# Performance work log

Measured on AMD Instinct MI355X. Metric: run time of the kernel, lower is better.

## Reference

```python
import jax, jax.numpy as jnp
import numpy as np

N = 50000       # nodes
E = 800000      # edges (before self-loops)
IN = 64         # in_channels
OUT = 64        # out_channels


def setup_inputs() -> dict:
    key = jax.random.key(0)
    ks = jax.random.split(key, 6)
    X = jax.random.normal(ks[0], (N, IN), jnp.float32)
    H = jax.random.normal(ks[1], (N, OUT), jnp.float32)
    edge_index = jax.random.randint(ks[2], (2, E), 0, N, dtype=jnp.int64)
    edge_weight = jax.random.uniform(ks[3], (E,), jnp.float32)
    fan_in = IN + OUT
    W1 = jax.random.normal(ks[4], (fan_in, 2 * OUT), jnp.float32) / np.sqrt(fan_in).astype(np.float32)
    b1 = jnp.ones((2 * OUT,), jnp.float32)   # TGCN sets graph_conv1.bias to ones
    W2 = jax.random.normal(ks[5], (fan_in, OUT), jnp.float32) / np.sqrt(fan_in).astype(np.float32)
    b2 = jnp.zeros((OUT,), jnp.float32)      # default GCNConv bias init
    return {"X": X, "H": H, "edge_index": edge_index, "edge_weight": edge_weight,
            "W1": W1, "b1": b1, "W2": W2, "b2": b2}


def _gcn_conv(x, W, b, src, dst, w, n):
    """PyG GCNConv: linear transform, add self-loops (fill=1, improved=False),
    symmetric deg^-1/2 normalization, scatter-add aggregation at dst, + bias."""
    x = x @ W                                   # [N, out]
    loop = jnp.arange(n, dtype=src.dtype)
    s = jnp.concatenate([src, loop])            # [E+N]
    d = jnp.concatenate([dst, loop])
    ww = jnp.concatenate([w, jnp.ones((n,), x.dtype)])
    deg = jax.ops.segment_sum(ww, d, num_segments=n)
    dinv = jnp.where(deg > 0, jax.lax.rsqrt(jnp.maximum(deg, 1e-12)), 0.0)
    norm = dinv[s] * ww * dinv[d]               # [E+N]
    msg = x[s] * norm[:, None]                  # gather + scale
    out = jax.ops.segment_sum(msg, d, num_segments=n)  # scatter-add at dst
    return out + b


def reference(X, H, edge_index, edge_weight, W1, b1, W2, b2):
    src, dst = edge_index[0], edge_index[1]
    n = X.shape[0]
    ru = jax.nn.sigmoid(_gcn_conv(jnp.concatenate([X, H], axis=1), W1, b1, src, dst, edge_weight, n))
    r, u = ru[:, :OUT], ru[:, OUT:]             # chunk into reset/update gates
    c = jnp.tanh(_gcn_conv(jnp.concatenate([X, H * r], axis=1), W2, b2, src, dst, edge_weight, n))
    return u * H + (1.0 - u) * c                # new hidden state [N, OUT]
```

## Files before the change

kernel.cpp:

```cpp
#include <hip/hip_runtime.h>
#include <hip/hip_bf16.h>
#include <hip/hip_fp16.h>

#define NN 50000
#define NE 800000
#define NBIN ((NN + 255) / 256)
#define PB ((NE + 1023) / 1024)
#define GB ((NN + 63) / 64)
#define MAXB 4864

typedef __attribute__((ext_vector_type(8))) short bf16x8;
typedef __attribute__((ext_vector_type(4))) float f32x4;
typedef __attribute__((ext_vector_type(2))) float f32x2;

__device__ __forceinline__ unsigned int f2bf(float x) {
    unsigned int u = __float_as_uint(x);
    return (u + 0x7FFFu + ((u >> 16) & 1u)) >> 16;
}
__device__ __forceinline__ float bf2f(unsigned int b) {
    return __uint_as_float(b << 16);
}
__device__ __forceinline__ float4 f8x4_dec(unsigned int u) {
    f32x2 lo = __builtin_amdgcn_cvt_pk_f32_fp8(u, false);
    f32x2 hi = __builtin_amdgcn_cvt_pk_f32_fp8(u, true);
    float4 r; r.x = lo[0]; r.y = lo[1]; r.z = hi[0]; r.w = hi[1];
    return r;
}
__device__ __forceinline__ unsigned int f8x4_enc(float a, float b, float c, float d) {
    int q = 0;
    q = __builtin_amdgcn_cvt_pk_fp8_f32(a, b, q, false);
    q = __builtin_amdgcn_cvt_pk_fp8_f32(c, d, q, true);
    return (unsigned int)q;
}

__global__ void k_wprep(const float* __restrict__ W1, const float* __restrict__ W2,
                        unsigned short* __restrict__ Wf1,
                        unsigned short* __restrict__ Wf2t,
                        unsigned short* __restrict__ Wf2b) {
    int i = blockIdx.x * 256 + threadIdx.x;
    if (i < 16384) {
        int j = i & 7, l = (i >> 3) & 63, n = (i >> 9) & 7, kc = i >> 12;
        int k = kc * 32 + ((l >> 4) << 3) + j;
        int col = (n << 4) + (l & 15);
        Wf1[i] = (unsigned short)f2bf(W1[k * 128 + col]);
    }
    if (i < 4096) {
        int j = i & 7, l = (i >> 3) & 63, n = (i >> 9) & 3, kc = i >> 11;
        int k = kc * 32 + ((l >> 4) << 3) + j;
        int col = (n << 4) + (l & 15);
        Wf2t[i] = (unsigned short)f2bf(W2[k * 64 + col]);
        Wf2b[i] = (unsigned short)f2bf(W2[(k + 64) * 64 + col]);
    }
}

template <int OUTC, int KC, int SRC, int OMODE>
__device__ __forceinline__ void mgemm_core(
    const float* __restrict__ X, const float* __restrict__ Hm,
    const unsigned int* __restrict__ RUb, const unsigned short* __restrict__ Wf,
    const float* __restrict__ Z2p, const float* __restrict__ dinv,
    unsigned short* __restrict__ outH, float* __restrict__ outF,
    int bid, unsigned short* aS, unsigned short* wS)
{
    constexpr int NT = OUTC / 16;
    const int tid = threadIdx.x;
    const int row0 = bid * 64;

    constexpr int WH = KC * NT * 64 * 8;
    {
        const uint4* Wg4 = reinterpret_cast<const uint4*>(Wf);
        uint4* wS4 = reinterpret_cast<uint4*>(wS);
        #pragma unroll
        for (int i = tid; i < WH / 8; i += 256) wS4[i] = Wg4[i];
    }
    #pragma unroll
    for (int i = tid; i < 64 * KC * 8; i += 256) {
        int row = i / (KC * 8), f4 = i % (KC * 8);
        int g = row0 + row;
        float4 v = {0.f, 0.f, 0.f, 0.f};
        if (g < NN) {
            if (SRC == 0) {
                v = (f4 < 16) ? reinterpret_cast<const float4*>(X)[g * 16 + f4]
                              : reinterpret_cast<const float4*>(Hm)[g * 16 + f4 - 16];
            } else if (SRC == 1) {
                v = reinterpret_cast<const float4*>(X)[g * 16 + f4];
            } else {
                v = reinterpret_cast<const float4*>(Hm)[g * 16 + f4];
                unsigned int r0 = RUb[g * 64 + 2 * f4];
                unsigned int r1 = RUb[g * 64 + 2 * f4 + 1];
                v.x *= bf2f(r0 & 0xFFFFu); v.y *= bf2f(r0 >> 16);
                v.z *= bf2f(r1 & 0xFFFFu); v.w *= bf2f(r1 >> 16);
            }
        }
        int k = f4 * 4;
        int kc = k >> 5, ko = k & 31;
        int l = (row & 15) | ((ko >> 3) << 4);
        int j0 = ko & 7;
        int m = row >> 4;
        uint2 pk;
        pk.x = f2bf(v.x) | (f2bf(v.y) << 16);
        pk.y = f2bf(v.z) | (f2bf(v.w) << 16);
        *reinterpret_cast<uint2*>(aS + (((m * KC + kc) * 64 + l) * 8 + j0)) = pk;
    }
    __syncthreads();

    const int wid = tid >> 6, l = tid & 63;
    f32x4 acc[NT];
    #pragma unroll
    for (int n = 0; n < NT; ++n) acc[n] = {0.f, 0.f, 0.f, 0.f};

    const bf16x8* aF = reinterpret_cast<const bf16x8*>(aS);
    const bf16x8* wF = reinterpret_cast<const bf16x8*>(wS);
    #pragma unroll
    for (int kc = 0; kc < KC; ++kc) {
        bf16x8 a = aF[(wid * KC + kc) * 64 + l];
        #pragma unroll
        for (int n = 0; n < NT; ++n) {
            bf16x8 b = wF[(kc * NT + n) * 64 + l];
            acc[n] = __builtin_amdgcn_mfma_f32_16x16x32_bf16(a, b, acc[n], 0, 0, 0);
        }
    }

    const int rbase = row0 + wid * 16 + ((l >> 4) << 2);
    const int cl = l & 15;
    float dv[4];
    if (OMODE == 2) {
        #pragma unroll
        for (int i = 0; i < 4; ++i) {
            int row = rbase + i;
            dv[i] = (row < NN) ? dinv[row] : 0.f;
        }
    }
    #pragma unroll
    for (int n = 0; n < NT; ++n) {
        #pragma unroll
        for (int i = 0; i < 4; ++i) {
            int row = rbase + i;
            if (row >= NN) continue;
            int col = n * 16 + cl;
            if (OMODE == 0) {
                outH[(size_t)row * OUTC + col] = (unsigned short)f2bf(acc[n][i]);
            } else if (OMODE == 1) {
                outF[(size_t)row * OUTC + col] = acc[n][i];
            } else {
                float a2 = (acc[n][i] + Z2p[(size_t)row * 64 + col]) * dv[i];
                outH[(size_t)row * 64 + col] = (unsigned short)f2bf(a2);
            }
        }
    }
}

__launch_bounds__(256)
__global__ void k_build(const float* __restrict__ X, const float* __restrict__ Hm,
                        const unsigned short* __restrict__ Wf1,
                        const unsigned short* __restrict__ Wf2t,
                        unsigned short* __restrict__ Z1b, float* __restrict__ Z2p,
                        const int* __restrict__ dst, int* __restrict__ HT) {
    __shared__ unsigned short aS[8192];
    __shared__ unsigned short wS[16384];
    const int bid = blockIdx.x;
    const int tid = threadIdx.x;
    if (bid < PB) {
        int* hist = reinterpret_cast<int*>(aS);
        for (int i = tid; i < NBIN; i += 256) hist[i] = 0;
        __syncthreads();
        const int base = bid * 1024 + tid;
        #pragma unroll
        for (int k = 0; k < 4; ++k) {
            int e = base + k * 256;
            if (e < NE) atomicAdd(&hist[dst[e] >> 8], 1);
        }
        __syncthreads();
        for (int i = tid; i < NBIN; i += 256) HT[i * PB + bid] = hist[i];
        return;
    }
    if (bid < PB + GB) {
        mgemm_core<128, 4, 0, 0>(X, Hm, nullptr, Wf1, nullptr, nullptr,
                                 Z1b, nullptr, bid - PB, aS, wS);
        return;
    }
    mgemm_core<64, 2, 1, 1>(X, Hm, nullptr, Wf2t, nullptr, nullptr,
                            nullptr, Z2p, bid - PB - GB, aS, wS);
}

__launch_bounds__(256)
__global__ void k_gemm2b(const float* __restrict__ X, const float* __restrict__ Hm,
                         const unsigned int* __restrict__ RUb,
                         const unsigned short* __restrict__ Wf2b,
                         const float* __restrict__ Z2p, const float* __restrict__ dinv,
                         unsigned short* __restrict__ Z2b) {
    __shared__ unsigned short aS[4096];
    __shared__ unsigned short wS[4096];
    mgemm_core<64, 2, 2, 2>(X, Hm, RUb, Wf2b, Z2p, dinv, Z2b, nullptr,
                            blockIdx.x, aS, wS);
}

__launch_bounds__(256)
__global__ void k_scanA1(const int* __restrict__ HT, int* __restrict__ within,
                         int* __restrict__ binTot) {
    __shared__ int lds[PB];
    __shared__ int sc[256];
    __shared__ int carryS;
    const int b = blockIdx.x, tid = threadIdx.x;
    if (tid == 0) carryS = 0;
    for (int i = tid; i < PB; i += 256) lds[i] = HT[b * PB + i];
    __syncthreads();
    for (int c0 = 0; c0 < PB; c0 += 256) {
        int i = c0 + tid;
        int v = (i < PB) ? lds[i] : 0;
        sc[tid] = v;
        __syncthreads();
        #pragma unroll
        for (int off = 1; off < 256; off <<= 1) {
            int t = (tid >= off) ? sc[tid - off] : 0;
            __syncthreads();
            sc[tid] += t;
            __syncthreads();
        }
        int carry = carryS;
        if (i < PB) lds[i] = carry + sc[tid] - v;
        __syncthreads();
        if (tid == 255) carryS = carry + sc[255];
        __syncthreads();
    }
    for (int i = tid; i < PB; i += 256) within[b * PB + i] = lds[i];
    if (tid == 0) binTot[b] = carryS;
}

__launch_bounds__(256)
__global__ void k_scatterA(const int* __restrict__ src, const int* __restrict__ dst,
                           const float* __restrict__ w, const int* __restrict__ binTot,
                           const int* __restrict__ within, uint2* __restrict__ rec) {
    __shared__ int bS[256];
    __shared__ int cur[NBIN];
    const int blk = blockIdx.x, tid = threadIdx.x;
    int bv = (tid < NBIN) ? binTot[tid] : 0;
    bS[tid] = bv;
    __syncthreads();
    #pragma unroll
    for (int off = 1; off < 256; off <<= 1) {
        int t = (tid >= off) ? bS[tid - off] : 0;
        __syncthreads();
        bS[tid] += t;
        __syncthreads();
    }
    if (tid < NBIN) cur[tid] = (bS[tid] - bv) + within[tid * PB + blk];
    __syncthreads();
    const int base = blk * 1024 + tid;
    #pragma unroll
    for (int k = 0; k < 4; ++k) {
        int e = base + k * 256;
        if (e < NE) {
            int d = dst[e];
            int pos = atomicAdd(&cur[d >> 8], 1);
            unsigned int hn = __half_as_ushort(__float2half(w[e]));
            uint2 r;
            r.x = (unsigned int)src[e] | (hn << 16);
            r.y = (unsigned int)d;
            rec[pos] = r;
        }
    }
}

__launch_bounds__(256)
__global__ void k_phase2(const uint2* __restrict__ rec, const int* __restrict__ binTot,
                         unsigned int* __restrict__ snP, int* __restrict__ start,
                         float* __restrict__ dinv, const uint2* __restrict__ Z1b,
                         unsigned int* __restrict__ Zf8) {
    __shared__ unsigned int rSn[MAXB];
    __shared__ unsigned char rLo[MAXB];
    __shared__ unsigned int outSn[MAXB];
    __shared__ int cnt[256];
    __shared__ int sc[256];
    __shared__ int lstart[256];
    __shared__ int cur[256];
    __shared__ float dls[256];
    const int b = blockIdx.x, tid = threadIdx.x;

    int bv = (tid < NBIN) ? binTot[tid] : 0;
    sc[tid] = bv;
    __syncthreads();
    #pragma unroll
    for (int off = 1; off < 256; off <<= 1) {
        int t = (tid >= off) ? sc[tid - off] : 0;
        __syncthreads();
        sc[tid] += t;
        __syncthreads();
    }
    const int e0 = (b == 0) ? 0 : sc[b - 1];
    int nE = sc[b] - e0;
    __syncthreads();
    if (nE > MAXB) nE = MAXB;

    cnt[tid] = 0;
    __syncthreads();
    for (int i = tid; i < nE; i += 256) {
        uint2 r = rec[e0 + i];
        rSn[i] = r.x;
        int lo = r.y & 255;
        rLo[i] = (unsigned char)lo;
        atomicAdd(&cnt[lo], 1);
    }
    __syncthreads();
    sc[tid] = cnt[tid];
    __syncthreads();
    #pragma unroll
    for (int off = 1; off < 256; off <<= 1) {
        int t = (tid >= off) ? sc[tid - off] : 0;
        __syncthreads();
        sc[tid] += t;
        __syncthreads();
    }
    lstart[tid] = sc[tid] - cnt[tid];
    cur[tid] = sc[tid] - cnt[tid];
    __syncthreads();
    const int node = b * 256 + tid;
    if (node <= NN) start[node] = e0 + lstart[tid];
    for (int i = tid; i < nE; i += 256) {
        int p = atomicAdd(&cur[rLo[i]], 1);
        outSn[p] = rSn[i];
    }
    __syncthreads();
    for (int i = tid; i < nE; i += 256) snP[e0 + i] = outSn[i];
    {
        int s0 = lstart[tid], c = cnt[tid];
        float sum = 0.f;
        for (int i = s0; i < s0 + c; ++i)
            sum += __half2float(__ushort_as_half((unsigned short)(outSn[i] >> 16)));
        float dv = rsqrtf(1.0f + sum);
        dls[tid] = dv;
        if (node < NN) dinv[node] = dv;
    }
    __syncthreads();
    const int nLoc = (NN - b * 256 < 256) ? (NN - b * 256) : 256;
    for (int i = tid; i < nLoc * 32; i += 256) {
        int l = i >> 5, j = i & 31;
        size_t g = (size_t)(b * 256 + l) * 32 + j;
        uint2 z = Z1b[g];
        float dv = dls[l];
        Zf8[g] = f8x4_enc(bf2f(z.x & 0xFFFFu) * dv, bf2f(z.x >> 16) * dv,
                          bf2f(z.y & 0xFFFFu) * dv, bf2f(z.y >> 16) * dv);
    }
}

__launch_bounds__(256)
__global__ void k_gather1(const int* __restrict__ start, const unsigned int* __restrict__ snP,
                          const unsigned int* __restrict__ Zf8, const float* __restrict__ dinv,
                          const float* __restrict__ bias, uint2* __restrict__ RUb2) {
    const int node = blockIdx.x * 8 + (threadIdx.x >> 5);
    const int l = threadIdx.x & 31;
    if (node >= NN) return;

    const int e0 = start[node], e1 = start[node + 1];
    float4 acc = f8x4_dec(Zf8[(size_t)node * 32 + l]);

    #define EFMA8(U, NM) { float4 zz = f8x4_dec(U); \
        acc.x += zz.x * (NM); acc.y += zz.y * (NM); \
        acc.z += zz.z * (NM); acc.w += zz.w * (NM); }

    int e = e0;
    for (; e + 8 <= e1; e += 8) {
        unsigned sn0 = snP[e],     sn1 = snP[e + 1], sn2 = snP[e + 2], sn3 = snP[e + 3];
        unsigned sn4 = snP[e + 4], sn5 = snP[e + 5], sn6 = snP[e + 6], sn7 = snP[e + 7];
        unsigned z0 = Zf8[(size_t)(sn0 & 0xFFFFu) * 32 + l];
        unsigned z1 = Zf8[(size_t)(sn1 & 0xFFFFu) * 32 + l];
        unsigned z2 = Zf8[(size_t)(sn2 & 0xFFFFu) * 32 + l];
        unsigned z3 = Zf8[(size_t)(sn3 & 0xFFFFu) * 32 + l];
        unsigned z4 = Zf8[(size_t)(sn4 & 0xFFFFu) * 32 + l];
        unsigned z5 = Zf8[(size_t)(sn5 & 0xFFFFu) * 32 + l];
        unsigned z6 = Zf8[(size_t)(sn6 & 0xFFFFu) * 32 + l];
        unsigned z7 = Zf8[(size_t)(sn7 & 0xFFFFu) * 32 + l];
        float n0 = __half2float(__ushort_as_half((unsigned short)(sn0 >> 16)));
        float n1 = __half2float(__ushort_as_half((unsigned short)(sn1 >> 16)));
        float n2 = __half2float(__ushort_as_half((unsigned short)(sn2 >> 16)));
        float n3 = __half2float(__ushort_as_half((unsigned short)(sn3 >> 16)));
        float n4 = __half2float(__ushort_as_half((unsigned short)(sn4 >> 16)));
        float n5 = __half2float(__ushort_as_half((unsigned short)(sn5 >> 16)));
        float n6 = __half2float(__ushort_as_half((unsigned short)(sn6 >> 16)));
        float n7 = __half2float(__ushort_as_half((unsigned short)(sn7 >> 16)));
        EFMA8(z0, n0) EFMA8(z1, n1) EFMA8(z2, n2) EFMA8(z3, n3)
        EFMA8(z4, n4) EFMA8(z5, n5) EFMA8(z6, n6) EFMA8(z7, n7)
    }
    if (e + 4 <= e1) {
        unsigned sn0 = snP[e], sn1 = snP[e + 1], sn2 = snP[e + 2], sn3 = snP[e + 3];
        unsigned z0 = Zf8[(size_t)(sn0 & 0xFFFFu) * 32 + l];
        unsigned z1 = Zf8[(size_t)(sn1 & 0xFFFFu) * 32 + l];
        unsigned z2 = Zf8[(size_t)(sn2 & 0xFFFFu) * 32 + l];
        unsigned z3 = Zf8[(size_t)(sn3 & 0xFFFFu) * 32 + l];
        float n0 = __half2float(__ushort_as_half((unsigned short)(sn0 >> 16)));
        float n1 = __half2float(__ushort_as_half((unsigned short)(sn1 >> 16)));
        float n2 = __half2float(__ushort_as_half((unsigned short)(sn2 >> 16)));
        float n3 = __half2float(__ushort_as_half((unsigned short)(sn3 >> 16)));
        EFMA8(z0, n0) EFMA8(z1, n1) EFMA8(z2, n2) EFMA8(z3, n3)
        e += 4;
    }
    for (; e < e1; ++e) {
        unsigned sn = snP[e];
        float nm = __half2float(__ushort_as_half((unsigned short)(sn >> 16)));
        unsigned z = Zf8[(size_t)(sn & 0xFFFFu) * 32 + l];
        EFMA8(z, nm)
    }
    #undef EFMA8

    const float dv = dinv[node];
    const int c = l * 4;
    float4 bb = *reinterpret_cast<const float4*>(bias + c);
    acc.x = acc.x * dv + bb.x; acc.y = acc.y * dv + bb.y;
    acc.z = acc.z * dv + bb.z; acc.w = acc.w * dv + bb.w;

    float4 o;
    o.x = 1.f / (1.f + expf(-acc.x));
    o.y = 1.f / (1.f + expf(-acc.y));
    o.z = 1.f / (1.f + expf(-acc.z));
    o.w = 1.f / (1.f + expf(-acc.w));
    uint2 pk;
    pk.x = f2bf(o.x) | (f2bf(o.y) << 16);
    pk.y = f2bf(o.z) | (f2bf(o.w) << 16);
    RUb2[(size_t)node * 32 + l] = pk;
}

__launch_bounds__(256)
__global__ void k_gather2(const int* __restrict__ start, const unsigned int* __restrict__ snP,
                          const uint2* __restrict__ Zb, const float* __restrict__ dinv,
                          const float* __restrict__ bias, const uint2* __restrict__ RUb2,
                          const float* __restrict__ Hm, float* __restrict__ out) {
    constexpr int GRP = 16;
    const int node = blockIdx.x * 16 + threadIdx.x / GRP;
    const int l = threadIdx.x % GRP;
    if (node >= NN) return;

    const int e0 = start[node], e1 = start[node + 1];

    uint2 zs = Zb[(size_t)node * GRP + l];
    float4 acc;
    acc.x = bf2f(zs.x & 0xFFFFu);
    acc.y = bf2f(zs.x >> 16);
    acc.z = bf2f(zs.y & 0xFFFFu);
    acc.w = bf2f(zs.y >> 16);

    #define EFMA(Z, NM) \
        acc.x += bf2f((Z).x & 0xFFFFu) * (NM); \
        acc.y += bf2f((Z).x >> 16) * (NM);     \
        acc.z += bf2f((Z).y & 0xFFFFu) * (NM); \
        acc.w += bf2f((Z).y >> 16) * (NM);

    int e = e0;
    for (; e + 8 <= e1; e += 8) {
        unsigned sn0 = snP[e],     sn1 = snP[e + 1], sn2 = snP[e + 2], sn3 = snP[e + 3];
        unsigned sn4 = snP[e + 4], sn5 = snP[e + 5], sn6 = snP[e + 6], sn7 = snP[e + 7];
        uint2 z0 = Zb[(size_t)(sn0 & 0xFFFFu) * GRP + l];
        uint2 z1 = Zb[(size_t)(sn1 & 0xFFFFu) * GRP + l];
        uint2 z2 = Zb[(size_t)(sn2 & 0xFFFFu) * GRP + l];
        uint2 z3 = Zb[(size_t)(sn3 & 0xFFFFu) * GRP + l];
        uint2 z4 = Zb[(size_t)(sn4 & 0xFFFFu) * GRP + l];
        uint2 z5 = Zb[(size_t)(sn5 & 0xFFFFu) * GRP + l];
        uint2 z6 = Zb[(size_t)(sn6 & 0xFFFFu) * GRP + l];
        uint2 z7 = Zb[(size_t)(sn7 & 0xFFFFu) * GRP + l];
        float n0 = __half2float(__ushort_as_half((unsigned short)(sn0 >> 16)));
        float n1 = __half2float(__ushort_as_half((unsigned short)(sn1 >> 16)));
        float n2 = __half2float(__ushort_as_half((unsigned short)(sn2 >> 16)));
        float n3 = __half2float(__ushort_as_half((unsigned short)(sn3 >> 16)));
        float n4 = __half2float(__ushort_as_half((unsigned short)(sn4 >> 16)));
        float n5 = __half2float(__ushort_as_half((unsigned short)(sn5 >> 16)));
        float n6 = __half2float(__ushort_as_half((unsigned short)(sn6 >> 16)));
        float n7 = __half2float(__ushort_as_half((unsigned short)(sn7 >> 16)));
        EFMA(z0, n0) EFMA(z1, n1) EFMA(z2, n2) EFMA(z3, n3)
        EFMA(z4, n4) EFMA(z5, n5) EFMA(z6, n6) EFMA(z7, n7)
    }
    if (e + 4 <= e1) {
        unsigned sn0 = snP[e], sn1 = snP[e + 1], sn2 = snP[e + 2], sn3 = snP[e + 3];
        uint2 z0 = Zb[(size_t)(sn0 & 0xFFFFu) * GRP + l];
        uint2 z1 = Zb[(size_t)(sn1 & 0xFFFFu) * GRP + l];
        uint2 z2 = Zb[(size_t)(sn2 & 0xFFFFu) * GRP + l];
        uint2 z3 = Zb[(size_t)(sn3 & 0xFFFFu) * GRP + l];
        float n0 = __half2float(__ushort_as_half((unsigned short)(sn0 >> 16)));
        float n1 = __half2float(__ushort_as_half((unsigned short)(sn1 >> 16)));
        float n2 = __half2float(__ushort_as_half((unsigned short)(sn2 >> 16)));
        float n3 = __half2float(__ushort_as_half((unsigned short)(sn3 >> 16)));
        EFMA(z0, n0) EFMA(z1, n1) EFMA(z2, n2) EFMA(z3, n3)
        e += 4;
    }
    for (; e < e1; ++e) {
        unsigned sn = snP[e];
        float nm = __half2float(__ushort_as_half((unsigned short)(sn >> 16)));
        uint2 z = Zb[(size_t)(sn & 0xFFFFu) * GRP + l];
        EFMA(z, nm)
    }
    #undef EFMA

    const float dv = dinv[node];
    const int c = l * 4;
    float4 bb = *reinterpret_cast<const float4*>(bias + c);
    acc.x = acc.x * dv + bb.x; acc.y = acc.y * dv + bb.y;
    acc.z = acc.z * dv + bb.z; acc.w = acc.w * dv + bb.w;

    uint2 uu = RUb2[(size_t)node * 32 + 16 + l];
    float u0 = bf2f(uu.x & 0xFFFFu), u1 = bf2f(uu.x >> 16);
    float u2 = bf2f(uu.y & 0xFFFFu), u3 = bf2f(uu.y >> 16);
    float4 h4 = *reinterpret_cast<const float4*>(Hm + (size_t)node * 64 + c);
    float4 o;
    o.x = u0 * h4.x + (1.f - u0) * tanhf(acc.x);
    o.y = u1 * h4.y + (1.f - u1) * tanhf(acc.y);
    o.z = u2 * h4.z + (1.f - u2) * tanhf(acc.z);
    o.w = u3 * h4.w + (1.f - u3) * tanhf(acc.w);
    *reinterpret_cast<float4*>(out + (size_t)node * 64 + c) = o;
}

extern "C" void kernel_launch(void* const* d_in, const int* in_sizes, int n_in,
                              void* d_out, int out_size, void* d_ws, size_t ws_size,
                              hipStream_t stream) {
    const float* X  = (const float*)d_in[0];
    const float* Hm = (const float*)d_in[1];
    const int*   ei = (const int*)d_in[2];
    const float* w  = (const float*)d_in[3];
    const float* W1 = (const float*)d_in[4];
    const float* b1 = (const float*)d_in[5];
    const float* W2 = (const float*)d_in[6];
    const float* b2 = (const float*)d_in[7];
    float* out = (float*)d_out;

    const int* src = ei;
    const int* dst = ei + NE;

    char* p = (char*)d_ws;
    uint2* rec   = (uint2*)p;  p += sizeof(uint2) * NE;
    uint2* Z1b   = (uint2*)p;  p += sizeof(uint2) * NN * 32;
    uint2* Z2b   = (uint2*)p;  p += sizeof(uint2) * NN * 16;
    uint2* RUb2  = (uint2*)p;  p += sizeof(uint2) * NN * 32;
    float* Z2p   = (float*)p;  p += sizeof(float) * NN * 64;
    float* dinv  = (float*)p;  p += sizeof(float) * NN;
    int*   start = (int*)p;    p += sizeof(int) * (NN + 1);
    int*   binTot   = (int*)p; p += sizeof(int) * (NBIN + 1);
    int*   HT       = (int*)p; p += sizeof(int) * NBIN * PB;
    int*   within   = (int*)p; p += sizeof(int) * NBIN * PB;
    unsigned int* snP = (unsigned int*)p; p += sizeof(unsigned int) * NE;
    unsigned int* Zf8 = (unsigned int*)p; p += sizeof(unsigned int) * NN * 32;
    unsigned short* Wf1  = (unsigned short*)p; p += sizeof(unsigned short) * 16384;
    unsigned short* Wf2t = (unsigned short*)p; p += sizeof(unsigned short) * 4096;
    unsigned short* Wf2b = (unsigned short*)p; p += sizeof(unsigned short) * 4096;

    k_wprep<<<64, 256, 0, stream>>>(W1, W2, Wf1, Wf2t, Wf2b);

    k_build<<<PB + 2 * GB, 256, 0, stream>>>(X, Hm, Wf1, Wf2t,
                                             (unsigned short*)Z1b, Z2p, dst, HT);

    k_scanA1<<<NBIN, 256, 0, stream>>>(HT, within, binTot);
    k_scatterA<<<PB, 256, 0, stream>>>(src, dst, w, binTot, within, rec);
    k_phase2<<<NBIN, 256, 0, stream>>>(rec, binTot, snP, start, dinv, Z1b, Zf8);

    k_gather1<<<(NN + 7) / 8, 256, 0, stream>>>(start, snP, Zf8, dinv, b1, RUb2);

    k_gemm2b<<<GB, 256, 0, stream>>>(X, Hm, (const unsigned int*)RUb2, Wf2b,
                                     Z2p, dinv, (unsigned short*)Z2b);
    k_gather2<<<(NN + 15) / 16, 256, 0, stream>>>(start, snP, Z2b, dinv, b2, RUb2, Hm, out);
}
```

Before: 122.4 us.

## Write unscaled fp8 Z1 from GEMM and apply source dinv per edge in gathers

```diff
diff --git a/kernel.cpp b/kernel.cpp
--- a/kernel.cpp
+++ b/kernel.cpp
@@ -25,12 +25,6 @@
     f32x2 hi = __builtin_amdgcn_cvt_pk_f32_fp8(u, true);
     float4 r; r.x = lo[0]; r.y = lo[1]; r.z = hi[0]; r.w = hi[1];
     return r;
-}
-__device__ __forceinline__ unsigned int f8x4_enc(float a, float b, float c, float d) {
-    int q = 0;
-    q = __builtin_amdgcn_cvt_pk_fp8_f32(a, b, q, false);
-    q = __builtin_amdgcn_cvt_pk_fp8_f32(c, d, q, true);
-    return (unsigned int)q;
 }
 
 __global__ void k_wprep(const float* __restrict__ W1, const float* __restrict__ W2,
@@ -57,8 +51,9 @@
 __device__ __forceinline__ void mgemm_core(
     const float* __restrict__ X, const float* __restrict__ Hm,
     const unsigned int* __restrict__ RUb, const unsigned short* __restrict__ Wf,
-    const float* __restrict__ Z2p, const float* __restrict__ dinv,
+    const float* __restrict__ addF,
     unsigned short* __restrict__ outH, float* __restrict__ outF,
+    unsigned char* __restrict__ outF8,
     int bid, unsigned short* aS, unsigned short* wS)
 {
     constexpr int NT = OUTC / 16;
@@ -122,14 +117,6 @@
 
     const int rbase = row0 + wid * 16 + ((l >> 4) << 2);
     const int cl = l & 15;
-    float dv[4];
-    if (OMODE == 2) {
-        #pragma unroll
-        for (int i = 0; i < 4; ++i) {
-            int row = rbase + i;
-            dv[i] = (row < NN) ? dinv[row] : 0.f;
-        }
-    }
     #pragma unroll
     for (int n = 0; n < NT; ++n) {
         #pragma unroll
@@ -137,13 +124,14 @@
             int row = rbase + i;
             if (row >= NN) continue;
             int col = n * 16 + cl;
-            if (OMODE == 0) {
-                outH[(size_t)row * OUTC + col] = (unsigned short)f2bf(acc[n][i]);
-            } else if (OMODE == 1) {
+            if (OMODE == 1) {
                 outF[(size_t)row * OUTC + col] = acc[n][i];
+            } else if (OMODE == 2) {
+                float a2 = acc[n][i] + addF[(size_t)row * OUTC + col];
+                outH[(size_t)row * OUTC + col] = (unsigned short)f2bf(a2);
             } else {
-                float a2 = (acc[n][i] + Z2p[(size_t)row * 64 + col]) * dv[i];
-                outH[(size_t)row * 64 + col] = (unsigned short)f2bf(a2);
+                int q = __builtin_amdgcn_cvt_pk_fp8_f32(acc[n][i], acc[n][i], 0, false);
+                outF8[(size_t)row * OUTC + col] = (unsigned char)(q & 0xFF);
             }
         }
     }
@@ -153,7 +141,7 @@
 __global__ void k_build(const float* __restrict__ X, const float* __restrict__ Hm,
                         const unsigned short* __restrict__ Wf1,
                         const unsigned short* __restrict__ Wf2t,
-                        unsigned short* __restrict__ Z1b, float* __restrict__ Z2p,
+                        unsigned char* __restrict__ Zf8, float* __restrict__ Z2p,
                         const int* __restrict__ dst, int* __restrict__ HT) {
     __shared__ unsigned short aS[8192];
     __shared__ unsigned short wS[16384];
@@ -174,23 +162,23 @@
         return;
     }
     if (bid < PB + GB) {
-        mgemm_core<128, 4, 0, 0>(X, Hm, nullptr, Wf1, nullptr, nullptr,
-                                 Z1b, nullptr, bid - PB, aS, wS);
+        mgemm_core<128, 4, 0, 3>(X, Hm, nullptr, Wf1, nullptr,
+                                 nullptr, nullptr, Zf8, bid - PB, aS, wS);
         return;
     }
-    mgemm_core<64, 2, 1, 1>(X, Hm, nullptr, Wf2t, nullptr, nullptr,
-                            nullptr, Z2p, bid - PB - GB, aS, wS);
+    mgemm_core<64, 2, 1, 1>(X, Hm, nullptr, Wf2t, nullptr,
+                            nullptr, Z2p, nullptr, bid - PB - GB, aS, wS);
 }
 
 __launch_bounds__(256)
 __global__ void k_gemm2b(const float* __restrict__ X, const float* __restrict__ Hm,
                          const unsigned int* __restrict__ RUb,
                          const unsigned short* __restrict__ Wf2b,
-                         const float* __restrict__ Z2p, const float* __restrict__ dinv,
+                         const float* __restrict__ Z2p,
                          unsigned short* __restrict__ Z2b) {
     __shared__ unsigned short aS[4096];
     __shared__ unsigned short wS[4096];
-    mgemm_core<64, 2, 2, 2>(X, Hm, RUb, Wf2b, Z2p, dinv, Z2b, nullptr,
+    mgemm_core<64, 2, 2, 2>(X, Hm, RUb, Wf2b, Z2p, Z2b, nullptr, nullptr,
                             blockIdx.x, aS, wS);
 }
 
@@ -264,8 +252,7 @@
 __launch_bounds__(256)
 __global__ void k_phase2(const uint2* __restrict__ rec, const int* __restrict__ binTot,
                          unsigned int* __restrict__ snP, int* __restrict__ start,
-                         float* __restrict__ dinv, const uint2* __restrict__ Z1b,
-                         unsigned int* __restrict__ Zf8) {
+                         float* __restrict__ dinv) {
     __shared__ unsigned int rSn[MAXB];
     __shared__ unsigned char rLo[MAXB];
     __shared__ unsigned int outSn[MAXB];
@@ -273,7 +260,6 @@
     __shared__ int sc[256];
     __shared__ int lstart[256];
     __shared__ int cur[256];
-    __shared__ float dls[256];
     const int b = blockIdx.x, tid = threadIdx.x;
 
     int bv = (tid < NBIN) ? binTot[tid] : 0;
@@ -326,19 +312,7 @@
         float sum = 0.f;
         for (int i = s0; i < s0 + c; ++i)
             sum += __half2float(__ushort_as_half((unsigned short)(outSn[i] >> 16)));
-        float dv = rsqrtf(1.0f + sum);
-        dls[tid] = dv;
-        if (node < NN) dinv[node] = dv;
-    }
-    __syncthreads();
-    const int nLoc = (NN - b * 256 < 256) ? (NN - b * 256) : 256;
-    for (int i = tid; i < nLoc * 32; i += 256) {
-        int l = i >> 5, j = i & 31;
-        size_t g = (size_t)(b * 256 + l) * 32 + j;
-        uint2 z = Z1b[g];
-        float dv = dls[l];
-        Zf8[g] = f8x4_enc(bf2f(z.x & 0xFFFFu) * dv, bf2f(z.x >> 16) * dv,
-                          bf2f(z.y & 0xFFFFu) * dv, bf2f(z.y >> 16) * dv);
+        if (node < NN) dinv[node] = rsqrtf(1.0f + sum);
     }
 }
 
@@ -351,11 +325,15 @@
     if (node >= NN) return;
 
     const int e0 = start[node], e1 = start[node + 1];
+    const float dvd = dinv[node];
     float4 acc = f8x4_dec(Zf8[(size_t)node * 32 + l]);
+    acc.x *= dvd; acc.y *= dvd; acc.z *= dvd; acc.w *= dvd;
 
     #define EFMA8(U, NM) { float4 zz = f8x4_dec(U); \
         acc.x += zz.x * (NM); acc.y += zz.y * (NM); \
         acc.z += zz.z * (NM); acc.w += zz.w * (NM); }
+    #define NMOF(SN) (dinv[(SN) & 0xFFFFu] * \
+        __half2float(__ushort_as_half((unsigned short)((SN) >> 16))))
 
     int e = e0;
     for (; e + 8 <= e1; e += 8) {
@@ -369,14 +347,8 @@
         unsigned z5 = Zf8[(size_t)(sn5 & 0xFFFFu) * 32 + l];
         unsigned z6 = Zf8[(size_t)(sn6 & 0xFFFFu) * 32 + l];
         unsigned z7 = Zf8[(size_t)(sn7 & 0xFFFFu) * 32 + l];
-        float n0 = __half2float(__ushort_as_half((unsigned short)(sn0 >> 16)));
-        float n1 = __half2float(__ushort_as_half((unsigned short)(sn1 >> 16)));
-        float n2 = __half2float(__ushort_as_half((unsigned short)(sn2 >> 16)));
-        float n3 = __half2float(__ushort_as_half((unsigned short)(sn3 >> 16)));
-        float n4 = __half2float(__ushort_as_half((unsigned short)(sn4 >> 16)));
-        float n5 = __half2float(__ushort_as_half((unsigned short)(sn5 >> 16)));
-        float n6 = __half2float(__ushort_as_half((unsigned short)(sn6 >> 16)));
-        float n7 = __half2float(__ushort_as_half((unsigned short)(sn7 >> 16)));
+        float n0 = NMOF(sn0), n1 = NMOF(sn1), n2 = NMOF(sn2), n3 = NMOF(sn3);
+        float n4 = NMOF(sn4), n5 = NMOF(sn5), n6 = NMOF(sn6), n7 = NMOF(sn7);
         EFMA8(z0, n0) EFMA8(z1, n1) EFMA8(z2, n2) EFMA8(z3, n3)
         EFMA8(z4, n4) EFMA8(z5, n5) EFMA8(z6, n6) EFMA8(z7, n7)
     }
@@ -386,26 +358,23 @@
         unsigned z1 = Zf8[(size_t)(sn1 & 0xFFFFu) * 32 + l];
         unsigned z2 = Zf8[(size_t)(sn2 & 0xFFFFu) * 32 + l];
         unsigned z3 = Zf8[(size_t)(sn3 & 0xFFFFu) * 32 + l];
-        float n0 = __half2float(__ushort_as_half((unsigned short)(sn0 >> 16)));
-        float n1 = __half2float(__ushort_as_half((unsigned short)(sn1 >> 16)));
-        float n2 = __half2float(__ushort_as_half((unsigned short)(sn2 >> 16)));
-        float n3 = __half2float(__ushort_as_half((unsigned short)(sn3 >> 16)));
+        float n0 = NMOF(sn0), n1 = NMOF(sn1), n2 = NMOF(sn2), n3 = NMOF(sn3);
         EFMA8(z0, n0) EFMA8(z1, n1) EFMA8(z2, n2) EFMA8(z3, n3)
         e += 4;
     }
     for (; e < e1; ++e) {
         unsigned sn = snP[e];
-        float nm = __half2float(__ushort_as_half((unsigned short)(sn >> 16)));
         unsigned z = Zf8[(size_t)(sn & 0xFFFFu) * 32 + l];
+        float nm = NMOF(sn);
         EFMA8(z, nm)
     }
     #undef EFMA8
-
-    const float dv = dinv[node];
+    #undef NMOF
+
     const int c = l * 4;
     float4 bb = *reinterpret_cast<const float4*>(bias + c);
-    acc.x = acc.x * dv + bb.x; acc.y = acc.y * dv + bb.y;
-    acc.z = acc.z * dv + bb.z; acc.w = acc.w * dv + bb.w;
+    acc.x = acc.x * dvd + bb.x; acc.y = acc.y * dvd + bb.y;
+    acc.z = acc.z * dvd + bb.z; acc.w = acc.w * dvd + bb.w;
 
     float4 o;
     o.x = 1.f / (1.f + expf(-acc.x));
@@ -429,19 +398,22 @@
     if (node >= NN) return;
 
     const int e0 = start[node], e1 = start[node + 1];
+    const float dvd = dinv[node];
 
     uint2 zs = Zb[(size_t)node * GRP + l];
     float4 acc;
-    acc.x = bf2f(zs.x & 0xFFFFu);
-    acc.y = bf2f(zs.x >> 16);
-    acc.z = bf2f(zs.y & 0xFFFFu);
-    acc.w = bf2f(zs.y >> 16);
+    acc.x = bf2f(zs.x & 0xFFFFu) * dvd;
+    acc.y = bf2f(zs.x >> 16) * dvd;
+    acc.z = bf2f(zs.y & 0xFFFFu) * dvd;
+    acc.w = bf2f(zs.y >> 16) * dvd;
 
     #define EFMA(Z, NM) \
         acc.x += bf2f((Z).x & 0xFFFFu) * (NM); \
         acc.y += bf2f((Z).x >> 16) * (NM);     \
         acc.z += bf2f((Z).y & 0xFFFFu) * (NM); \
         acc.w += bf2f((Z).y >> 16) * (NM);
+    #define NMOF(SN) (dinv[(SN) & 0xFFFFu] * \
+        __half2float(__ushort_as_half((unsigned short)((SN) >> 16))))
 
     int e = e0;
     for (; e + 8 <= e1; e += 8) {
@@ -455,14 +427,8 @@
         uint2 z5 = Zb[(size_t)(sn5 & 0xFFFFu) * GRP + l];
         uint2 z6 = Zb[(size_t)(sn6 & 0xFFFFu) * GRP + l];
         uint2 z7 = Zb[(size_t)(sn7 & 0xFFFFu) * GRP + l];
-        float n0 = __half2float(__ushort_as_half((unsigned short)(sn0 >> 16)));
-        float n1 = __half2float(__ushort_as_half((unsigned short)(sn1 >> 16)));
-        float n2 = __half2float(__ushort_as_half((unsigned short)(sn2 >> 16)));
-        float n3 = __half2float(__ushort_as_half((unsigned short)(sn3 >> 16)));
-        float n4 = __half2float(__ushort_as_half((unsigned short)(sn4 >> 16)));
-        float n5 = __half2float(__ushort_as_half((unsigned short)(sn5 >> 16)));
-        float n6 = __half2float(__ushort_as_half((unsigned short)(sn6 >> 16)));
-        float n7 = __half2float(__ushort_as_half((unsigned short)(sn7 >> 16)));
+        float n0 = NMOF(sn0), n1 = NMOF(sn1), n2 = NMOF(sn2), n3 = NMOF(sn3);
+        float n4 = NMOF(sn4), n5 = NMOF(sn5), n6 = NMOF(sn6), n7 = NMOF(sn7);
         EFMA(z0, n0) EFMA(z1, n1) EFMA(z2, n2) EFMA(z3, n3)
         EFMA(z4, n4) EFMA(z5, n5) EFMA(z6, n6) EFMA(z7, n7)
     }
@@ -472,26 +438,23 @@
         uint2 z1 = Zb[(size_t)(sn1 & 0xFFFFu) * GRP + l];
         uint2 z2 = Zb[(size_t)(sn2 & 0xFFFFu) * GRP + l];
         uint2 z3 = Zb[(size_t)(sn3 & 0xFFFFu) * GRP + l];
-        float n0 = __half2float(__ushort_as_half((unsigned short)(sn0 >> 16)));
-        float n1 = __half2float(__ushort_as_half((unsigned short)(sn1 >> 16)));
-        float n2 = __half2float(__ushort_as_half((unsigned short)(sn2 >> 16)));
-        float n3 = __half2float(__ushort_as_half((unsigned short)(sn3 >> 16)));
+        float n0 = NMOF(sn0), n1 = NMOF(sn1), n2 = NMOF(sn2), n3 = NMOF(sn3);
         EFMA(z0, n0) EFMA(z1, n1) EFMA(z2, n2) EFMA(z3, n3)
         e += 4;
     }
     for (; e < e1; ++e) {
         unsigned sn = snP[e];
-        float nm = __half2float(__ushort_as_half((unsigned short)(sn >> 16)));
         uint2 z = Zb[(size_t)(sn & 0xFFFFu) * GRP + l];
+        float nm = NMOF(sn);
         EFMA(z, nm)
     }
     #undef EFMA
-
-    const float dv = dinv[node];
+    #undef NMOF
+
     const int c = l * 4;
     float4 bb = *reinterpret_cast<const float4*>(bias + c);
-    acc.x = acc.x * dv + bb.x; acc.y = acc.y * dv + bb.y;
-    acc.z = acc.z * dv + bb.z; acc.w = acc.w * dv + bb.w;
+    acc.x = acc.x * dvd + bb.x; acc.y = acc.y * dvd + bb.y;
+    acc.z = acc.z * dvd + bb.z; acc.w = acc.w * dvd + bb.w;
 
     uint2 uu = RUb2[(size_t)node * 32 + 16 + l];
     float u0 = bf2f(uu.x & 0xFFFFu), u1 = bf2f(uu.x >> 16);
@@ -523,7 +486,6 @@
 
     char* p = (char*)d_ws;
     uint2* rec   = (uint2*)p;  p += sizeof(uint2) * NE;
-    uint2* Z1b   = (uint2*)p;  p += sizeof(uint2) * NN * 32;
     uint2* Z2b   = (uint2*)p;  p += sizeof(uint2) * NN * 16;
     uint2* RUb2  = (uint2*)p;  p += sizeof(uint2) * NN * 32;
     float* Z2p   = (float*)p;  p += sizeof(float) * NN * 64;
@@ -541,15 +503,15 @@
     k_wprep<<<64, 256, 0, stream>>>(W1, W2, Wf1, Wf2t, Wf2b);
 
     k_build<<<PB + 2 * GB, 256, 0, stream>>>(X, Hm, Wf1, Wf2t,
-                                             (unsigned short*)Z1b, Z2p, dst, HT);
+                                             (unsigned char*)Zf8, Z2p, dst, HT);
 
     k_scanA1<<<NBIN, 256, 0, stream>>>(HT, within, binTot);
     k_scatterA<<<PB, 256, 0, stream>>>(src, dst, w, binTot, within, rec);
-    k_phase2<<<NBIN, 256, 0, stream>>>(rec, binTot, snP, start, dinv, Z1b, Zf8);
+    k_phase2<<<NBIN, 256, 0, stream>>>(rec, binTot, snP, start, dinv);
 
     k_gather1<<<(NN + 7) / 8, 256, 0, stream>>>(start, snP, Zf8, dinv, b1, RUb2);
 
-    k_gemm2b<<<GB, 256, 0, stream>>>(X, Hm, (const unsigned int*)RUb2, Wf2b,
-                                     Z2p, dinv, (unsigned short*)Z2b);
+    k_gemm2b<<<GB, 256, 0, stream>>>(X, Hm, (const unsigned int*)RUb2, Wf2b, Z2p,
+                                     (unsigned short*)Z2b);
     k_gather2<<<(NN + 15) / 16, 256, 0, stream>>>(start, snP, Z2b, dinv, b2, RUb2, Hm, out);
 }
```

Result: faster. 114.7 us (-6.3%).
